# Kernel tuning notes

Hardware: AMD Instinct MI355X
Metric: run time of the kernel (lower is better)

The kernel has to match this reference:

```python
import jax, jax.numpy as jnp
import numpy as np

NUM_NODES = 50000
NUM_EDGES = 800000
NUM_FEATURES = 128
HIDDEN = 128
NUM_CLASSES = 40


def setup_inputs() -> dict:
    key = jax.random.key(0)
    ks = jax.random.split(key, 10)
    x = jax.random.normal(ks[0], (NUM_NODES, NUM_FEATURES), dtype=jnp.float32)
    edge_index = jax.random.randint(ks[1], (2, NUM_EDGES), 0, NUM_NODES, dtype=jnp.int32)
    def glorot(k, fan_in, fan_out):
        s = jnp.sqrt(6.0 / (fan_in + fan_out))
        return jax.random.uniform(k, (fan_in, fan_out), jnp.float32, -s, s)
    return {
        "x": x,
        "edge_index": edge_index,
        "W1": glorot(ks[2], NUM_FEATURES, HIDDEN), "b1": jnp.zeros((HIDDEN,), jnp.float32),
        "W2": glorot(ks[3], HIDDEN, HIDDEN),       "b2": jnp.zeros((HIDDEN,), jnp.float32),
        "W3": glorot(ks[4], HIDDEN, HIDDEN),       "b3": jnp.zeros((HIDDEN,), jnp.float32),
        "Wc": glorot(ks[5], HIDDEN, NUM_CLASSES),  "bc": jnp.zeros((NUM_CLASSES,), jnp.float32),
    }


def _gcn_norm(edge_index, num_nodes, dtype):
    # add self-loops, symmetric normalization D^{-1/2} (A+I) D^{-1/2}
    loops = jnp.arange(num_nodes, dtype=edge_index.dtype)
    src = jnp.concatenate([edge_index[0], loops])
    dst = jnp.concatenate([edge_index[1], loops])
    deg = jax.ops.segment_sum(jnp.ones_like(dst, dtype=dtype), dst, num_segments=num_nodes)
    dinv = jnp.where(deg > 0, jax.lax.rsqrt(deg), 0.0)
    norm = dinv[src] * dinv[dst]  # [E + N]
    return src, dst, norm


def _gcn_conv(h, W, b, src, dst, norm, num_nodes):
    h = h @ W                                  # [N, out]
    msg = h[src] * norm[:, None]               # gather + scale  [E+N, out]
    agg = jax.ops.segment_sum(msg, dst, num_segments=num_nodes)
    return agg + b


def reference(x, edge_index, W1, b1, W2, b2, W3, b3, Wc, bc):
    N = x.shape[0]
    src, dst, norm = _gcn_norm(edge_index, N, x.dtype)
    h = jax.nn.relu(_gcn_conv(x, W1, b1, src, dst, norm, N))
    h = jax.nn.relu(_gcn_conv(h, W2, b2, src, dst, norm, N))
    h = jax.nn.relu(_gcn_conv(h, W3, b3, src, dst, norm, N))
    out = h @ Wc + bc
    return (out, h)
```

## Files before the change

kernel.cpp:

```cpp
#include <hip/hip_runtime.h>

typedef float f32x4 __attribute__((ext_vector_type(4)));
typedef short s16x8 __attribute__((ext_vector_type(8)));

__device__ __forceinline__ float us2f(unsigned short u) {
    union { unsigned int i; float f; } v;
    v.i = ((unsigned int)u) << 16;
    return v.f;
}
__device__ __forceinline__ unsigned short f2us(float f) {
    union { unsigned int i; float f; } v; v.f = f;
    unsigned int r = v.i + 0x7fff + ((v.i >> 16) & 1);
    return (unsigned short)(r >> 16);
}

__global__ void k_wprep(const float* __restrict__ W1, const float* __restrict__ W2,
                        const float* __restrict__ W3, const float* __restrict__ Wc,
                        unsigned short* __restrict__ img, int* __restrict__ bcnt) {
    int b = blockIdx.x >> 7;
    int n = threadIdx.x;
    if (b >= 4) { bcnt[n] = 0; bcnt[n + 128] = 0; return; }
    int k = blockIdx.x & 127;
    unsigned short *H, *L;
    float f;
    if (b < 3) {
        const float* W = (b == 0) ? W1 : ((b == 1) ? W2 : W3);
        H = img + b * 32768; L = H + 16384;
        f = W[k * 128 + n];
    } else {
        if (n >= 48) return;
        H = img + 3 * 32768; L = H + 6144;
        f = (n < 40) ? Wc[k * 40 + n] : 0.f;
    }
    unsigned short h = f2us(f);
    unsigned short l = f2us(f - us2f(h));
    int idx = n * 128 + ((((k >> 3) ^ (n & 15))) << 3) + (k & 7);
    H[idx] = h; L[idx] = l;
}

__global__ __launch_bounds__(256) void k_hist(const int* __restrict__ dst, int E, int chunk,
                                              int* __restrict__ bcnt) {
    __shared__ int cnt[256];
    int t = threadIdx.x;
    cnt[t] = 0; __syncthreads();
    int s = blockIdx.x * chunk;
    int e = s + chunk; if (e > E) e = E;
    for (int i = s + t; i < e; i += 256) atomicAdd(&cnt[dst[i] >> 8], 1);
    __syncthreads();
    if (cnt[t]) atomicAdd(&bcnt[t], cnt[t]);
}

__global__ void k_bscan(const int* __restrict__ bcnt, int* __restrict__ bofs,
                        int* __restrict__ gcur) {
    __shared__ int s[256];
    int t = threadIdx.x;
    int v = bcnt[t];
    s[t] = v; __syncthreads();
    for (int off = 1; off < 256; off <<= 1) {
        int x = (t >= off) ? s[t - off] : 0;
        __syncthreads();
        s[t] += x;
        __syncthreads();
    }
    int ex = s[t] - v;
    bofs[t] = ex; gcur[t] = ex;
    if (t == 255) bofs[256] = s[255];
}

__global__ __launch_bounds__(256) void k_scatter1(const int* __restrict__ src,
                                                  const int* __restrict__ dst, int E, int chunk,
                                                  int* __restrict__ gcur,
                                                  unsigned int* __restrict__ pk) {
    __shared__ int cnt[256];
    int t = threadIdx.x;
    cnt[t] = 0; __syncthreads();
    int s = blockIdx.x * chunk;
    int e = s + chunk; if (e > E) e = E;
    for (int i = s + t; i < e; i += 256) atomicAdd(&cnt[dst[i] >> 8], 1);
    __syncthreads();
    int base = atomicAdd(&gcur[t], cnt[t]);
    cnt[t] = base;
    __syncthreads();
    for (int i = s + t; i < e; i += 256) {
        int d = dst[i];
        int slot = atomicAdd(&cnt[d >> 8], 1);
        pk[slot] = ((unsigned int)src[i] << 8) | (unsigned int)(d & 255);
    }
}

__global__ __launch_bounds__(256) void k_degscan(const unsigned int* __restrict__ pk,
                                                 const int* __restrict__ bofs,
                                                 int* __restrict__ row_ptr,
                                                 int* __restrict__ bsum,
                                                 float* __restrict__ dinv, int N) {
    __shared__ int cnt[256];
    __shared__ int s[256];
    int t = threadIdx.x, b = blockIdx.x;
    cnt[t] = 0; __syncthreads();
    int s0 = bofs[b], s1 = bofs[b + 1];
    for (int i = s0 + t; i < s1; i += 256) atomicAdd(&cnt[pk[i] & 255], 1);
    __syncthreads();
    int v = cnt[t];
    s[t] = v; __syncthreads();
    for (int off = 1; off < 256; off <<= 1) {
        int x = (t >= off) ? s[t - off] : 0;
        __syncthreads();
        s[t] += x;
        __syncthreads();
    }
    int node = (b << 8) + t;
    if (node < N) {
        row_ptr[node] = s[t] - v;
        dinv[node] = rsqrtf((float)(v + 1));
    }
    if (t == 255) bsum[b] = s[255];
}

__global__ void k_scan2(int* __restrict__ bsum, int nb) {
    __shared__ int s[256];
    int t = threadIdx.x;
    int v = (t < nb) ? bsum[t] : 0;
    s[t] = v; __syncthreads();
    for (int off = 1; off < 256; off <<= 1) {
        int x = (t >= off) ? s[t - off] : 0;
        __syncthreads();
        s[t] += x;
        __syncthreads();
    }
    if (t < nb) bsum[t] = s[t] - v;
}

__global__ __launch_bounds__(256) void k_scatter2(const unsigned int* __restrict__ pk,
                                                  const int* __restrict__ bofs,
                                                  int* __restrict__ row_ptr,
                                                  const int* __restrict__ bsum,
                                                  int* __restrict__ csr, int N, int E) {
    __shared__ int cur[256];
    int t = threadIdx.x, b = blockIdx.x;
    int node = (b << 8) + t;
    int rp = 0;
    if (node < N) {
        rp = row_ptr[node] + bsum[b];
        row_ptr[node] = rp;
    }
    cur[t] = rp;
    __syncthreads();
    int s = bofs[b], e = bofs[b + 1];
    for (int i = s + t; i < e; i += 256) {
        unsigned int v = pk[i];
        int slot = atomicAdd(&cur[v & 255], 1);
        csr[slot] = (int)(v >> 8);
    }
    if (node == N - 1) row_ptr[N] = E;
}

template <bool ABF16>
__global__ __launch_bounds__(256) void k_gemm128m(const void* __restrict__ Ap,
                                                  const unsigned short* __restrict__ img,
                                                  const float* __restrict__ dinv,
                                                  unsigned short* __restrict__ M, int N) {
    __shared__ __align__(16) unsigned short WsH[16384];
    __shared__ __align__(16) unsigned short WsL[16384];
    int t = threadIdx.x;
    {
        const uint4* s = (const uint4*)img;
        uint4* dH = (uint4*)WsH; uint4* dL = (uint4*)WsL;
#pragma unroll
        for (int i = 0; i < 8; i++) dH[t + i * 256] = s[t + i * 256];
#pragma unroll
        for (int i = 0; i < 8; i++) dL[t + i * 256] = s[2048 + t + i * 256];
    }
    __syncthreads();

    int w = t >> 6, lane = t & 63;
    int m = lane & 15, q = lane >> 4;
    int row0 = blockIdx.x * 64 + w * 16;
    int gr = row0 + m;
    int grc = (gr < N) ? gr : (N - 1);
    const float* A32 = (const float*)Ap + (size_t)grc * 128;
    const unsigned short* A16 = (const unsigned short*)Ap + (size_t)grc * 128;
    int nbase = m * 128;

    f32x4 acc[8];
#pragma unroll
    for (int cb = 0; cb < 8; cb++) { acc[cb][0]=0.f; acc[cb][1]=0.f; acc[cb][2]=0.f; acc[cb][3]=0.f; }

#pragma unroll
    for (int ks = 0; ks < 4; ks++) {
        union { unsigned short u[8]; s16x8 v; } ah, al;
        if constexpr (ABF16) {
            ah.v = *(const s16x8*)&A16[ks * 32 + q * 8];
        } else {
            float4 f0 = ((const float4*)A32)[ks * 8 + q * 2];
            float4 f1 = ((const float4*)A32)[ks * 8 + q * 2 + 1];
            float fv[8] = {f0.x, f0.y, f0.z, f0.w, f1.x, f1.y, f1.z, f1.w};
#pragma unroll
            for (int j = 0; j < 8; j++) {
                unsigned short h = f2us(fv[j]);
                ah.u[j] = h;
                al.u[j] = f2us(fv[j] - us2f(h));
            }
        }
        int koff = (((ks * 4 + q) ^ m) & 15) << 3;
#pragma unroll
        for (int cb = 0; cb < 8; cb++) {
            int o = cb * 2048 + nbase + koff;
            s16x8 wh = *(const s16x8*)&WsH[o];
            s16x8 wl = *(const s16x8*)&WsL[o];
            acc[cb] = __builtin_amdgcn_mfma_f32_16x16x32_bf16(ah.v, wh, acc[cb], 0, 0, 0);
            acc[cb] = __builtin_amdgcn_mfma_f32_16x16x32_bf16(ah.v, wl, acc[cb], 0, 0, 0);
            if constexpr (!ABF16)
                acc[cb] = __builtin_amdgcn_mfma_f32_16x16x32_bf16(al.v, wh, acc[cb], 0, 0, 0);
        }
    }

#pragma unroll
    for (int r = 0; r < 4; r++) {
        int grow = row0 + q * 4 + r;
        if (grow < N) {
            float dv = dinv[grow];
#pragma unroll
            for (int cb = 0; cb < 8; cb++)
                M[(size_t)grow * 128 + cb * 16 + m] = f2us(acc[cb][r] * dv);
        }
    }
}

__global__ __launch_bounds__(256) void k_gemm40m(const float* __restrict__ A,
                                                 const unsigned short* __restrict__ img,
                                                 const float* __restrict__ bc,
                                                 float* __restrict__ out, int N) {
    __shared__ __align__(16) unsigned short WsH[6144];
    __shared__ __align__(16) unsigned short WsL[6144];
    int t = threadIdx.x;
    {
        const uint4* s = (const uint4*)img;
        uint4* dH = (uint4*)WsH; uint4* dL = (uint4*)WsL;
#pragma unroll
        for (int i = 0; i < 3; i++) dH[t + i * 256] = s[t + i * 256];
#pragma unroll
        for (int i = 0; i < 3; i++) dL[t + i * 256] = s[768 + t + i * 256];
    }
    __syncthreads();

    int w = t >> 6, lane = t & 63;
    int m = lane & 15, q = lane >> 4;
    int row0 = blockIdx.x * 64 + w * 16;
    int gr = row0 + m;
    int grc = (gr < N) ? gr : (N - 1);
    const float4* Arow = (const float4*)(A + (size_t)grc * 128);
    int nbase = m * 128;

    f32x4 acc[3];
#pragma unroll
    for (int cb = 0; cb < 3; cb++) { acc[cb][0]=0.f; acc[cb][1]=0.f; acc[cb][2]=0.f; acc[cb][3]=0.f; }

#pragma unroll
    for (int ks = 0; ks < 4; ks++) {
        float4 f0 = Arow[ks * 8 + q * 2];
        float4 f1 = Arow[ks * 8 + q * 2 + 1];
        float fv[8] = {f0.x, f0.y, f0.z, f0.w, f1.x, f1.y, f1.z, f1.w};
        union { unsigned short u[8]; s16x8 v; } ah, al;
#pragma unroll
        for (int j = 0; j < 8; j++) {
            unsigned short h = f2us(fv[j]);
            ah.u[j] = h;
            al.u[j] = f2us(fv[j] - us2f(h));
        }
        int koff = (((ks * 4 + q) ^ m) & 15) << 3;
#pragma unroll
        for (int cb = 0; cb < 3; cb++) {
            int o = cb * 2048 + nbase + koff;
            s16x8 wh = *(const s16x8*)&WsH[o];
            s16x8 wl = *(const s16x8*)&WsL[o];
            acc[cb] = __builtin_amdgcn_mfma_f32_16x16x32_bf16(ah.v, wh, acc[cb], 0, 0, 0);
            acc[cb] = __builtin_amdgcn_mfma_f32_16x16x32_bf16(ah.v, wl, acc[cb], 0, 0, 0);
            acc[cb] = __builtin_amdgcn_mfma_f32_16x16x32_bf16(al.v, wh, acc[cb], 0, 0, 0);
        }
    }

#pragma unroll
    for (int r = 0; r < 4; r++) {
        int grow = row0 + q * 4 + r;
        if (grow < N) {
#pragma unroll
            for (int cb = 0; cb < 3; cb++) {
                int col = cb * 16 + m;
                if (col < 40) out[(size_t)grow * 40 + col] = acc[cb][r] + bc[col];
            }
        }
    }
}

template <bool OUT_BF16>
__global__ __launch_bounds__(256) void k_gather(const unsigned short* __restrict__ M,
                                                const int* __restrict__ csr,
                                                const int* __restrict__ row_ptr,
                                                const float* __restrict__ dinv,
                                                const float* __restrict__ bias,
                                                void* __restrict__ H, int N) {
    int w    = (blockIdx.x << 2) + (threadIdx.x >> 6);
    int lane = threadIdx.x & 63;
    if (w >= N) return;
    int g  = lane >> 4;
    int sl = lane & 15;

    const uint4* M16 = (const uint4*)M;
    float acc[8];
#pragma unroll
    for (int i = 0; i < 8; i++) acc[i] = 0.f;

    auto accum = [&](uint4 tv) {
        unsigned int uu[4] = {tv.x, tv.y, tv.z, tv.w};
#pragma unroll
        for (int i = 0; i < 4; i++) {
            acc[2 * i]     += us2f((unsigned short)(uu[i] & 0xffffu));
            acc[2 * i + 1] += us2f((unsigned short)(uu[i] >> 16));
        }
    };

    if (g == 0) accum(M16[(size_t)w * 16 + sl]);

    int s0 = row_ptr[w], s1 = row_ptr[w + 1];
    for (int base = s0; base < s1; base += 64) {
        int n = s1 - base; if (n > 64) n = 64;
        int idx = (lane < n) ? csr[base + lane] : 0;
        int full = n >> 2;
        int rem  = n & 3;
        int j = 0;
        for (; j + 8 <= full; j += 8) {
            int u0 = __shfl(idx, (j + 0) * 4 + g);
            int u1 = __shfl(idx, (j + 1) * 4 + g);
            int u2 = __shfl(idx, (j + 2) * 4 + g);
            int u3 = __shfl(idx, (j + 3) * 4 + g);
            int u4 = __shfl(idx, (j + 4) * 4 + g);
            int u5 = __shfl(idx, (j + 5) * 4 + g);
            int u6 = __shfl(idx, (j + 6) * 4 + g);
            int u7 = __shfl(idx, (j + 7) * 4 + g);
            uint4 t0 = M16[(size_t)u0 * 16 + sl];
            uint4 t1 = M16[(size_t)u1 * 16 + sl];
            uint4 t2 = M16[(size_t)u2 * 16 + sl];
            uint4 t3 = M16[(size_t)u3 * 16 + sl];
            uint4 t4 = M16[(size_t)u4 * 16 + sl];
            uint4 t5 = M16[(size_t)u5 * 16 + sl];
            uint4 t6 = M16[(size_t)u6 * 16 + sl];
            uint4 t7 = M16[(size_t)u7 * 16 + sl];
            accum(t0); accum(t1); accum(t2); accum(t3);
            accum(t4); accum(t5); accum(t6); accum(t7);
        }
        for (; j + 4 <= full; j += 4) {
            int u0 = __shfl(idx, (j + 0) * 4 + g);
            int u1 = __shfl(idx, (j + 1) * 4 + g);
            int u2 = __shfl(idx, (j + 2) * 4 + g);
            int u3 = __shfl(idx, (j + 3) * 4 + g);
            uint4 t0 = M16[(size_t)u0 * 16 + sl];
            uint4 t1 = M16[(size_t)u1 * 16 + sl];
            uint4 t2 = M16[(size_t)u2 * 16 + sl];
            uint4 t3 = M16[(size_t)u3 * 16 + sl];
            accum(t0); accum(t1); accum(t2); accum(t3);
        }
        for (; j < full; j++) {
            int u = __shfl(idx, j * 4 + g);
            accum(M16[(size_t)u * 16 + sl]);
        }
        int ur = __shfl(idx, ((full << 2) + g) & 63);
        if (g < rem) accum(M16[(size_t)ur * 16 + sl]);
    }

#pragma unroll
    for (int i = 0; i < 8; i++) {
        acc[i] += __shfl_xor(acc[i], 16);
        acc[i] += __shfl_xor(acc[i], 32);
    }

    float dv = dinv[w];
    const float4* b4 = (const float4*)bias;
    float4 b0 = b4[sl * 2], b1 = b4[sl * 2 + 1];
    float o[8];
    o[0] = fmaxf(fmaf(dv, acc[0], b0.x), 0.f);
    o[1] = fmaxf(fmaf(dv, acc[1], b0.y), 0.f);
    o[2] = fmaxf(fmaf(dv, acc[2], b0.z), 0.f);
    o[3] = fmaxf(fmaf(dv, acc[3], b0.w), 0.f);
    o[4] = fmaxf(fmaf(dv, acc[4], b1.x), 0.f);
    o[5] = fmaxf(fmaf(dv, acc[5], b1.y), 0.f);
    o[6] = fmaxf(fmaf(dv, acc[6], b1.z), 0.f);
    o[7] = fmaxf(fmaf(dv, acc[7], b1.w), 0.f);

    if (g == 0) {
        if constexpr (OUT_BF16) {
            uint4 p;
            p.x = (unsigned int)f2us(o[0]) | ((unsigned int)f2us(o[1]) << 16);
            p.y = (unsigned int)f2us(o[2]) | ((unsigned int)f2us(o[3]) << 16);
            p.z = (unsigned int)f2us(o[4]) | ((unsigned int)f2us(o[5]) << 16);
            p.w = (unsigned int)f2us(o[6]) | ((unsigned int)f2us(o[7]) << 16);
            ((uint4*)H)[(size_t)w * 16 + sl] = p;
        } else {
            float4* H4 = (float4*)H;
            H4[(size_t)w * 32 + sl * 2]     = make_float4(o[0], o[1], o[2], o[3]);
            H4[(size_t)w * 32 + sl * 2 + 1] = make_float4(o[4], o[5], o[6], o[7]);
        }
    }
}

extern "C" void kernel_launch(void* const* d_in, const int* in_sizes, int n_in,
                              void* d_out, int out_size, void* d_ws, size_t ws_size,
                              hipStream_t stream) {
    const float* x  = (const float*)d_in[0];
    const int*   ei = (const int*)d_in[1];
    const float* W1 = (const float*)d_in[2];
    const float* b1 = (const float*)d_in[3];
    const float* W2 = (const float*)d_in[4];
    const float* b2 = (const float*)d_in[5];
    const float* W3 = (const float*)d_in[6];
    const float* b3 = (const float*)d_in[7];
    const float* Wc = (const float*)d_in[8];
    const float* bc = (const float*)d_in[9];

    const int N = in_sizes[0] / 128;
    const int E = in_sizes[1] / 2;
    const int* src = ei;
    const int* dst = ei + E;

    char* ws = (char*)d_ws;
    size_t off = 0;
    auto alloc = [&](size_t bytes) -> void* {
        void* p = ws + off;
        off = (off + bytes + 255) & ~(size_t)255;
        return p;
    };
    unsigned short* Mbuf = (unsigned short*)alloc((size_t)N * 128 * 2);
    unsigned short* Hb   = (unsigned short*)alloc((size_t)N * 128 * 2);
    unsigned int* pk     = (unsigned int*)alloc((size_t)E * 4);
    unsigned short* img  = (unsigned short*)alloc((3 * 32768 + 2 * 6144) * 2);
    float* dinv    = (float*)alloc((size_t)N * 4);
    int*   row_ptr = (int*)alloc((size_t)(N + 1) * 4);
    int*   csr     = (int*)alloc((size_t)E * 4);
    int*   bcnt    = (int*)alloc(256 * 4);
    int*   bofs    = (int*)alloc(257 * 4);
    int*   gcur    = (int*)alloc(256 * 4);
    int*   bsum    = (int*)alloc(256 * 4);

    float* out  = (float*)d_out;
    float* hbuf = out + (size_t)N * 40;

    const int nb  = (N + 255) / 256;
    const int NB  = (N + 255) >> 8;
    const int G1  = 256;
    const int chunk = (E + G1 - 1) / G1;

    k_wprep<<<513, 128, 0, stream>>>(W1, W2, W3, Wc, img, bcnt);

    k_hist<<<G1, 256, 0, stream>>>(dst, E, chunk, bcnt);
    k_bscan<<<1, 256, 0, stream>>>(bcnt, bofs, gcur);
    k_scatter1<<<G1, 256, 0, stream>>>(src, dst, E, chunk, gcur, pk);
    k_degscan<<<NB, 256, 0, stream>>>(pk, bofs, row_ptr, bsum, dinv, N);
    k_scan2<<<1, 256, 0, stream>>>(bsum, nb);
    k_scatter2<<<NB, 256, 0, stream>>>(pk, bofs, row_ptr, bsum, csr, N, E);

    const int gb  = (N + 63) / 64;
    const int gab = (N + 3) / 4;

    k_gemm128m<false><<<gb, 256, 0, stream>>>(x, img, dinv, Mbuf, N);
    k_gather<true><<<gab, 256, 0, stream>>>(Mbuf, csr, row_ptr, dinv, b1, Hb, N);
    k_gemm128m<true><<<gb, 256, 0, stream>>>(Hb, img + 32768, dinv, Mbuf, N);
    k_gather<true><<<gab, 256, 0, stream>>>(Mbuf, csr, row_ptr, dinv, b2, Hb, N);
    k_gemm128m<true><<<gb, 256, 0, stream>>>(Hb, img + 2 * 32768, dinv, Mbuf, N);
    k_gather<false><<<gab, 256, 0, stream>>>(Mbuf, csr, row_ptr, dinv, b3, hbuf, N);
    k_gemm40m<<<gb, 256, 0, stream>>>(hbuf, img + 3 * 32768, bc, out, N);
}
```

Measured before the change: 294.7 us.

## Fuse classifier GEMM into final gather kernel and drop 8-way unroll

Removes the separate classifier GEMM kernel and computes the 40-class output inside the last aggregation kernel. Each block stages a transposed Wc in shared memory and computes the products with FP32 FMAs and shuffle reductions. This saves one launch and one read of the hidden features, and the hidden output is now written with nontemporal stores. The gather loop also loses its 8-wide unrolled stage, which lowers register use but may reduce memory-level parallelism. Every block now pays for a 20KB shared-memory load and transpose of Wc, and the scalar FMA classifier adds ALU work per node.

New measurement: 396.1 us. 1.34x slower.

```diff
diff --git a/kernel.cpp b/kernel.cpp
--- a/kernel.cpp
+++ b/kernel.cpp
@@ -226,73 +226,6 @@
     }
 }
 
-__global__ __launch_bounds__(256) void k_gemm40m(const float* __restrict__ A,
-                                                 const unsigned short* __restrict__ img,
-                                                 const float* __restrict__ bc,
-                                                 float* __restrict__ out, int N) {
-    __shared__ __align__(16) unsigned short WsH[6144];
-    __shared__ __align__(16) unsigned short WsL[6144];
-    int t = threadIdx.x;
-    {
-        const uint4* s = (const uint4*)img;
-        uint4* dH = (uint4*)WsH; uint4* dL = (uint4*)WsL;
-#pragma unroll
-        for (int i = 0; i < 3; i++) dH[t + i * 256] = s[t + i * 256];
-#pragma unroll
-        for (int i = 0; i < 3; i++) dL[t + i * 256] = s[768 + t + i * 256];
-    }
-    __syncthreads();
-
-    int w = t >> 6, lane = t & 63;
-    int m = lane & 15, q = lane >> 4;
-    int row0 = blockIdx.x * 64 + w * 16;
-    int gr = row0 + m;
-    int grc = (gr < N) ? gr : (N - 1);
-    const float4* Arow = (const float4*)(A + (size_t)grc * 128);
-    int nbase = m * 128;
-
-    f32x4 acc[3];
-#pragma unroll
-    for (int cb = 0; cb < 3; cb++) { acc[cb][0]=0.f; acc[cb][1]=0.f; acc[cb][2]=0.f; acc[cb][3]=0.f; }
-
-#pragma unroll
-    for (int ks = 0; ks < 4; ks++) {
-        float4 f0 = Arow[ks * 8 + q * 2];
-        float4 f1 = Arow[ks * 8 + q * 2 + 1];
-        float fv[8] = {f0.x, f0.y, f0.z, f0.w, f1.x, f1.y, f1.z, f1.w};
-        union { unsigned short u[8]; s16x8 v; } ah, al;
-#pragma unroll
-        for (int j = 0; j < 8; j++) {
-            unsigned short h = f2us(fv[j]);
-            ah.u[j] = h;
-            al.u[j] = f2us(fv[j] - us2f(h));
-        }
-        int koff = (((ks * 4 + q) ^ m) & 15) << 3;
-#pragma unroll
-        for (int cb = 0; cb < 3; cb++) {
-            int o = cb * 2048 + nbase + koff;
-            s16x8 wh = *(const s16x8*)&WsH[o];
-            s16x8 wl = *(const s16x8*)&WsL[o];
-            acc[cb] = __builtin_amdgcn_mfma_f32_16x16x32_bf16(ah.v, wh, acc[cb], 0, 0, 0);
-            acc[cb] = __builtin_amdgcn_mfma_f32_16x16x32_bf16(ah.v, wl, acc[cb], 0, 0, 0);
-            acc[cb] = __builtin_amdgcn_mfma_f32_16x16x32_bf16(al.v, wh, acc[cb], 0, 0, 0);
-        }
-    }
-
-#pragma unroll
-    for (int r = 0; r < 4; r++) {
-        int grow = row0 + q * 4 + r;
-        if (grow < N) {
-#pragma unroll
-            for (int cb = 0; cb < 3; cb++) {
-                int col = cb * 16 + m;
-                if (col < 40) out[(size_t)grow * 40 + col] = acc[cb][r] + bc[col];
-            }
-        }
-    }
-}
-
-template <bool OUT_BF16>
 __global__ __launch_bounds__(256) void k_gather(const unsigned short* __restrict__ M,
                                                 const int* __restrict__ csr,
                                                 const int* __restrict__ row_ptr,
@@ -328,26 +261,6 @@
         int full = n >> 2;
         int rem  = n & 3;
         int j = 0;
-        for (; j + 8 <= full; j += 8) {
-            int u0 = __shfl(idx, (j + 0) * 4 + g);
-            int u1 = __shfl(idx, (j + 1) * 4 + g);
-            int u2 = __shfl(idx, (j + 2) * 4 + g);
-            int u3 = __shfl(idx, (j + 3) * 4 + g);
-            int u4 = __shfl(idx, (j + 4) * 4 + g);
-            int u5 = __shfl(idx, (j + 5) * 4 + g);
-            int u6 = __shfl(idx, (j + 6) * 4 + g);
-            int u7 = __shfl(idx, (j + 7) * 4 + g);
-            uint4 t0 = M16[(size_t)u0 * 16 + sl];
-            uint4 t1 = M16[(size_t)u1 * 16 + sl];
-            uint4 t2 = M16[(size_t)u2 * 16 + sl];
-            uint4 t3 = M16[(size_t)u3 * 16 + sl];
-            uint4 t4 = M16[(size_t)u4 * 16 + sl];
-            uint4 t5 = M16[(size_t)u5 * 16 + sl];
-            uint4 t6 = M16[(size_t)u6 * 16 + sl];
-            uint4 t7 = M16[(size_t)u7 * 16 + sl];
-            accum(t0); accum(t1); accum(t2); accum(t3);
-            accum(t4); accum(t5); accum(t6); accum(t7);
-        }
         for (; j + 4 <= full; j += 4) {
             int u0 = __shfl(idx, (j + 0) * 4 + g);
             int u1 = __shfl(idx, (j + 1) * 4 + g);
@@ -387,19 +300,129 @@
     o[7] = fmaxf(fmaf(dv, acc[7], b1.w), 0.f);
 
     if (g == 0) {
-        if constexpr (OUT_BF16) {
-            uint4 p;
-            p.x = (unsigned int)f2us(o[0]) | ((unsigned int)f2us(o[1]) << 16);
-            p.y = (unsigned int)f2us(o[2]) | ((unsigned int)f2us(o[3]) << 16);
-            p.z = (unsigned int)f2us(o[4]) | ((unsigned int)f2us(o[5]) << 16);
-            p.w = (unsigned int)f2us(o[6]) | ((unsigned int)f2us(o[7]) << 16);
-            ((uint4*)H)[(size_t)w * 16 + sl] = p;
-        } else {
-            float4* H4 = (float4*)H;
-            H4[(size_t)w * 32 + sl * 2]     = make_float4(o[0], o[1], o[2], o[3]);
-            H4[(size_t)w * 32 + sl * 2 + 1] = make_float4(o[4], o[5], o[6], o[7]);
-        }
-    }
+        uint4 p;
+        p.x = (unsigned int)f2us(o[0]) | ((unsigned int)f2us(o[1]) << 16);
+        p.y = (unsigned int)f2us(o[2]) | ((unsigned int)f2us(o[3]) << 16);
+        p.z = (unsigned int)f2us(o[4]) | ((unsigned int)f2us(o[5]) << 16);
+        p.w = (unsigned int)f2us(o[6]) | ((unsigned int)f2us(o[7]) << 16);
+        ((uint4*)H)[(size_t)w * 16 + sl] = p;
+    }
+}
+
+__global__ __launch_bounds__(256) void k_gather_cls(const unsigned short* __restrict__ M,
+                                                    const int* __restrict__ csr,
+                                                    const int* __restrict__ row_ptr,
+                                                    const float* __restrict__ dinv,
+                                                    const float* __restrict__ bias,
+                                                    const float* __restrict__ Wc,
+                                                    const float* __restrict__ bc,
+                                                    float* __restrict__ hbuf,
+                                                    float* __restrict__ out, int N) {
+    __shared__ float WcT[40 * 129];
+    __shared__ float bcs[40];
+    int t = threadIdx.x;
+    for (int i = t; i < 5120; i += 256) {
+        int c = i >> 7;
+        int k = i & 127;
+        WcT[c * 129 + k] = Wc[k * 40 + c];
+    }
+    if (t < 40) bcs[t] = bc[t];
+    __syncthreads();
+
+    int w    = (blockIdx.x << 2) + (t >> 6);
+    int lane = t & 63;
+    if (w >= N) return;
+    int g  = lane >> 4;
+    int sl = lane & 15;
+
+    const uint4* M16 = (const uint4*)M;
+    float acc[8];
+#pragma unroll
+    for (int i = 0; i < 8; i++) acc[i] = 0.f;
+
+    auto accum = [&](uint4 tv) {
+        unsigned int uu[4] = {tv.x, tv.y, tv.z, tv.w};
+#pragma unroll
+        for (int i = 0; i < 4; i++) {
+            acc[2 * i]     += us2f((unsigned short)(uu[i] & 0xffffu));
+            acc[2 * i + 1] += us2f((unsigned short)(uu[i] >> 16));
+        }
+    };
+
+    if (g == 0) accum(M16[(size_t)w * 16 + sl]);
+
+    int s0 = row_ptr[w], s1 = row_ptr[w + 1];
+    for (int base = s0; base < s1; base += 64) {
+        int n = s1 - base; if (n > 64) n = 64;
+        int idx = (lane < n) ? csr[base + lane] : 0;
+        int full = n >> 2;
+        int rem  = n & 3;
+        int j = 0;
+        for (; j + 4 <= full; j += 4) {
+            int u0 = __shfl(idx, (j + 0) * 4 + g);
+            int u1 = __shfl(idx, (j + 1) * 4 + g);
+            int u2 = __shfl(idx, (j + 2) * 4 + g);
+            int u3 = __shfl(idx, (j + 3) * 4 + g);
+            uint4 t0 = M16[(size_t)u0 * 16 + sl];
+            uint4 t1 = M16[(size_t)u1 * 16 + sl];
+            uint4 t2 = M16[(size_t)u2 * 16 + sl];
+            uint4 t3 = M16[(size_t)u3 * 16 + sl];
+            accum(t0); accum(t1); accum(t2); accum(t3);
+        }
+        for (; j < full; j++) {
+            int u = __shfl(idx, j * 4 + g);
+            accum(M16[(size_t)u * 16 + sl]);
+        }
+        int ur = __shfl(idx, ((full << 2) + g) & 63);
+        if (g < rem) accum(M16[(size_t)ur * 16 + sl]);
+    }
+
+#pragma unroll
+    for (int i = 0; i < 8; i++) {
+        acc[i] += __shfl_xor(acc[i], 16);
+        acc[i] += __shfl_xor(acc[i], 32);
+    }
+
+    float dv = dinv[w];
+    const float4* b4 = (const float4*)bias;
+    float4 b0 = b4[sl * 2], b1 = b4[sl * 2 + 1];
+    float o[8];
+    o[0] = fmaxf(fmaf(dv, acc[0], b0.x), 0.f);
+    o[1] = fmaxf(fmaf(dv, acc[1], b0.y), 0.f);
+    o[2] = fmaxf(fmaf(dv, acc[2], b0.z), 0.f);
+    o[3] = fmaxf(fmaf(dv, acc[3], b0.w), 0.f);
+    o[4] = fmaxf(fmaf(dv, acc[4], b1.x), 0.f);
+    o[5] = fmaxf(fmaf(dv, acc[5], b1.y), 0.f);
+    o[6] = fmaxf(fmaf(dv, acc[6], b1.z), 0.f);
+    o[7] = fmaxf(fmaf(dv, acc[7], b1.w), 0.f);
+
+    if (g == 0) {
+        f32x4 p0 = {o[0], o[1], o[2], o[3]};
+        f32x4 p1 = {o[4], o[5], o[6], o[7]};
+        __builtin_nontemporal_store(p0, (f32x4*)&hbuf[(size_t)w * 128 + sl * 8]);
+        __builtin_nontemporal_store(p1, (f32x4*)&hbuf[(size_t)w * 128 + sl * 8 + 4]);
+    }
+
+    float part[10];
+#pragma unroll
+    for (int c = 0; c < 10; c++) part[c] = 0.f;
+#pragma unroll
+    for (int c = 0; c < 10; c++) {
+        const float* wr = &WcT[(g * 10 + c) * 129 + sl * 8];
+#pragma unroll
+        for (int j = 0; j < 8; j++) part[c] = fmaf(o[j], wr[j], part[c]);
+    }
+#pragma unroll
+    for (int c = 0; c < 10; c++) {
+        part[c] += __shfl_xor(part[c], 1);
+        part[c] += __shfl_xor(part[c], 2);
+        part[c] += __shfl_xor(part[c], 4);
+        part[c] += __shfl_xor(part[c], 8);
+    }
+    float val = part[0];
+#pragma unroll
+    for (int c = 1; c < 10; c++) val = (sl == c) ? part[c] : val;
+    if (sl < 10) out[(size_t)w * 40 + g * 10 + sl] = val + bcs[g * 10 + sl];
 }
 
 extern "C" void kernel_launch(void* const* d_in, const int* in_sizes, int n_in,
@@ -461,10 +484,9 @@
     const int gab = (N + 3) / 4;
 
     k_gemm128m<false><<<gb, 256, 0, stream>>>(x, img, dinv, Mbuf, N);
-    k_gather<true><<<gab, 256, 0, stream>>>(Mbuf, csr, row_ptr, dinv, b1, Hb, N);
+    k_gather<<<gab, 256, 0, stream>>>(Mbuf, csr, row_ptr, dinv, b1, Hb, N);
     k_gemm128m<true><<<gb, 256, 0, stream>>>(Hb, img + 32768, dinv, Mbuf, N);
-    k_gather<true><<<gab, 256, 0, stream>>>(Mbuf, csr, row_ptr, dinv, b2, Hb, N);
+    k_gather<<<gab, 256, 0, stream>>>(Mbuf, csr, row_ptr, dinv, b2, Hb, N);
     k_gemm128m<true><<<gb, 256, 0, stream>>>(Hb, img + 2 * 32768, dinv, Mbuf, N);
-    k_gather<false><<<gab, 256, 0, stream>>>(Mbuf, csr, row_ptr, dinv, b3, hbuf, N);
-    k_gemm40m<<<gb, 256, 0, stream>>>(hbuf, img + 3 * 32768, bc, out, N);
-}
+    k_gather_cls<<<gab, 256, 0, stream>>>(Mbuf, csr, row_ptr, dinv, b3, Wc, bc, hbuf, out, N);
+}
```
